# Kernel tuning notes

Measured on AMD Instinct MI355X. Metric: run time of the kernel, lower is better.

## Reference

```python
import jax, jax.numpy as jnp
import numpy as np

E, D, H, R = 8, 2048, 8192, 64   # experts, d_model(in=out), hidden, rank
N = 4096                          # tokens (batch*seq)


def setup_inputs() -> dict:
    key = jax.random.key(0)
    ks = jax.random.split(key, 8)
    f32 = jnp.float32
    x = jax.random.normal(ks[0], (N, D), f32)
    # Stacked low-rank expert params: expert i = relu(x@u1@v1+b1) @ u2 @ v2 + b2
    u1 = jax.random.normal(ks[1], (E, D, R), f32) / np.float32(np.sqrt(D))
    v1 = jax.random.normal(ks[2], (E, R, H), f32) / np.float32(np.sqrt(R))
    b1 = jnp.zeros((E, H), f32)
    u2 = jax.random.normal(ks[3], (E, H, R), f32) / np.float32(np.sqrt(H))
    v2 = jax.random.normal(ks[4], (E, R, D), f32) / np.float32(np.sqrt(R))
    b2 = jnp.zeros((E, D), f32)
    # gate = nn.Linear(D, E): weight [E, D], bias [E]
    gate_w = jax.random.normal(ks[5], (E, D), f32) / np.float32(np.sqrt(D))
    gate_b = jnp.zeros((E,), f32)
    return dict(x=x, u1=u1, v1=v1, b1=b1, u2=u2, v2=v2, b2=b2,
                gate_w=gate_w, gate_b=gate_b)


def reference(x, u1, v1, b1, u2, v2, b2, gate_w, gate_b):
    # --- routing: softmax gate, top-2, renormalize ---
    logits = x @ gate_w.T + gate_b                      # [N, E]
    probs = jax.nn.softmax(logits, axis=-1)
    top_p, top_i = jax.lax.top_k(probs, 2)              # [N, 2]
    top_p = top_p / jnp.sum(top_p, axis=-1, keepdims=True)
    # combine weight per (token, expert): zero unless expert in top-2
    w = jnp.sum(jax.nn.one_hot(top_i, E, dtype=x.dtype) * top_p[..., None], axis=1)  # [N, E]

    # --- experts: low-rank MLP applied per expert, weighted accumulate ---
    def body(acc, params):
        u1e, v1e, b1e, u2e, v2e, b2e, we = params       # we: [N]
        h = jax.nn.relu((x @ u1e) @ v1e + b1e)          # [N, H]
        y = (h @ u2e) @ v2e + b2e                       # [N, D]
        return acc + we[:, None] * y, None

    out, _ = jax.lax.scan(body, jnp.zeros_like(x), (u1, v1, b1, u2, v2, b2, w.T))
    return out
```

## Files before the change

### kernel.cpp

```cpp
#include <hip/hip_runtime.h>
#include <hip/hip_bf16.h>

#define E 8
#define D 2048
#define H 8192
#define R 64
#define NTOK 4096
#define HSPLIT 4
#define HPER (H / HSPLIT)

typedef __attribute__((ext_vector_type(8))) short bf16x8;
typedef __attribute__((ext_vector_type(4))) float f32x4;

__device__ __forceinline__ unsigned short f2b(float f){
  union { __hip_bfloat16 h; unsigned short u; } cv;
  cv.h = __float2bfloat16(f);
  return cv.u;
}
__device__ __forceinline__ float b2f(unsigned short u){
  union { unsigned int i; float f; } cv; cv.i = ((unsigned int)u) << 16; return cv.f;
}

__device__ __forceinline__ bf16x8 ldfrag(const unsigned short* base, int row0, int k0,
                                         int pitch, int lane){
  return *reinterpret_cast<const bf16x8*>(base + (row0 + (lane & 15)) * pitch
                                          + k0 + ((lane >> 4) << 3));
}

__global__ __launch_bounds__(256) void pack_tr(const float* __restrict__ src,
                                               unsigned short* __restrict__ dst,
                                               int RS, int CS){
  int e = blockIdx.z;
  const float* s = src + (size_t)e * RS * CS;
  unsigned short* d = dst + (size_t)e * RS * CS;
  int c0 = blockIdx.x * 64, r0 = blockIdx.y * 64;
  int l = threadIdx.x & 63, cb = (threadIdx.x >> 6) * 16;
  int r = r0 + l;
  const float4* sp = reinterpret_cast<const float4*>(s + (size_t)r * CS + c0 + cb);
  float v[16];
  #pragma unroll
  for (int q = 0; q < 4; ++q){
    float4 t = sp[q];
    v[q*4] = t.x; v[q*4+1] = t.y; v[q*4+2] = t.z; v[q*4+3] = t.w;
  }
  #pragma unroll
  for (int j = 0; j < 16; ++j)
    d[(size_t)(c0 + cb + j) * RS + r] = f2b(v[j]);
}

__global__ __launch_bounds__(256) void gate_kernel(
    const float* __restrict__ x, const float* __restrict__ gw,
    const float* __restrict__ gb, int* __restrict__ tsl,
    unsigned short* __restrict__ xb)
{
  int wid  = threadIdx.x >> 6;
  int lane = threadIdx.x & 63;
  int n0 = blockIdx.x * 8 + wid * 2;

  float acc[2][E];
  #pragma unroll
  for (int t = 0; t < 2; ++t)
    #pragma unroll
    for (int e = 0; e < E; ++e) acc[t][e] = 0.f;

  for (int i = 0; i < D / 256; ++i){
    int dd = i * 256 + lane * 4;
    float4 xv[2];
    #pragma unroll
    for (int t = 0; t < 2; ++t){
      xv[t] = *reinterpret_cast<const float4*>(x + (size_t)(n0 + t) * D + dd);
      unsigned short o[4] = { f2b(xv[t].x), f2b(xv[t].y), f2b(xv[t].z), f2b(xv[t].w) };
      *reinterpret_cast<ushort4*>(xb + (size_t)(n0 + t) * D + dd) = *reinterpret_cast<ushort4*>(o);
    }
    #pragma unroll
    for (int e = 0; e < E; ++e){
      float4 g = *reinterpret_cast<const float4*>(gw + (size_t)e * D + dd);
      #pragma unroll
      for (int t = 0; t < 2; ++t)
        acc[t][e] += xv[t].x * g.x + xv[t].y * g.y + xv[t].z * g.z + xv[t].w * g.w;
    }
  }

  #pragma unroll
  for (int t = 0; t < 2; ++t){
    #pragma unroll
    for (int e = 0; e < E; ++e){
      float v = acc[t][e];
      for (int off = 32; off; off >>= 1) v += __shfl_xor(v, off, 64);
      acc[t][e] = v + gb[e];
    }
    if (lane == 0){
      int n = n0 + t;
      float l0 = -1e30f, l1 = -1e30f; int i0 = 0, i1 = 0;
      #pragma unroll
      for (int e = 0; e < E; ++e){
        float v = acc[t][e];
        if (v > l0){ l1 = l0; i1 = i0; l0 = v; i0 = e; }
        else if (v > l1){ l1 = v; i1 = e; }
      }
      float tt = expf(l1 - l0);
      float w0 = 1.f / (1.f + tt);
      float w1 = tt * w0;
      int* ts = tsl + n * 8;
      ts[0] = i0; ts[2] = __float_as_int(w0);
      ts[3] = i1; ts[5] = __float_as_int(w1);
    }
  }
}

__global__ __launch_bounds__(256) void route_kernel(
    int* __restrict__ tsl, int* __restrict__ cnt, int* __restrict__ lst)
{
  int wid  = threadIdx.x >> 6;
  int lane = threadIdx.x & 63;
  int tok  = blockIdx.x * 256 + wid * 64 + lane;
  int* ts = tsl + tok * 8;
  int i0 = ts[0], i1 = ts[3];
  unsigned long long below = (1ULL << lane) - 1ULL;

  #pragma unroll
  for (int e = 0; e < E; ++e){
    unsigned long long m0 = __ballot(i0 == e);
    unsigned long long m1 = __ballot(i1 == e);
    int c0  = __popcll(m0);
    int tot = c0 + __popcll(m1);
    int base = 0;
    if (lane == 0 && tot) base = atomicAdd(&cnt[e], tot);
    base = __shfl(base, 0, 64);
    if (i0 == e){
      int p = base + __popcll(m0 & below);
      lst[e * NTOK + p] = tok;  ts[1] = p;
    }
    if (i1 == e){
      int p = base + c0 + __popcll(m1 & below);
      lst[e * NTOK + p] = tok;  ts[4] = p;
    }
  }
}

__global__ __launch_bounds__(256) void t1_kernel(
    const unsigned short* __restrict__ xb, const unsigned short* __restrict__ u1p,
    const int* __restrict__ cnt, const int* __restrict__ lst,
    unsigned short* __restrict__ T1buf)
{
  int e = blockIdx.y;
  int nc = cnt[e];
  int t0 = blockIdx.x * 64;
  if (t0 >= nc) return;

  __shared__ int s_tok[64];
  __shared__ unsigned short Xs[64 * 136];
  __shared__ unsigned short U1s[64 * 136];
  int tid = threadIdx.x, w = tid >> 6, lane = tid & 63;

  if (tid < 64) s_tok[tid] = lst[e * NTOK + min(t0 + tid, nc - 1)];
  __syncthreads();

  int m = (w & 3) * 16;
  f32x4 z = {0.f, 0.f, 0.f, 0.f};
  f32x4 acc[4] = {z, z, z, z};

  for (int kc = 0; kc < D; kc += 128){
    __syncthreads();
    #pragma unroll
    for (int s = 0; s < 4; ++s){
      int id = tid + s * 256;
      int rr = id >> 4, c = (id & 15) * 8;
      *reinterpret_cast<bf16x8*>(&Xs[rr * 136 + c]) =
        *reinterpret_cast<const bf16x8*>(&xb[(size_t)s_tok[rr] * D + kc + c]);
      *reinterpret_cast<bf16x8*>(&U1s[rr * 136 + c]) =
        *reinterpret_cast<const bf16x8*>(&u1p[((size_t)e * R + rr) * D + kc + c]);
    }
    __syncthreads();
    #pragma unroll
    for (int j = 0; j < 4; ++j)
      #pragma unroll
      for (int ks = 0; ks < 4; ++ks)
        acc[j] = __builtin_amdgcn_mfma_f32_16x16x32_bf16(
            ldfrag(Xs, m, ks * 32, 136, lane),
            ldfrag(U1s, j * 16, ks * 32, 136, lane), acc[j], 0, 0, 0);
  }
  #pragma unroll
  for (int j = 0; j < 4; ++j){
    int col = j * 16 + (lane & 15);
    #pragma unroll
    for (int q = 0; q < 4; ++q){
      int row = m + ((lane >> 4) << 2) + q;
      T1buf[((size_t)e * NTOK + t0 + row) * R + col] = f2b(acc[j][q]);
    }
  }
}

__global__ __launch_bounds__(512, 4) void mid_kernel(
    const unsigned short* __restrict__ T1buf, const unsigned short* __restrict__ v1p,
    const unsigned short* __restrict__ u2p, const float* __restrict__ b1,
    const int* __restrict__ cnt, float* __restrict__ T2acc)
{
  int e = blockIdx.z;
  int nc = cnt[e];
  int t0 = blockIdx.x * 64;
  if (t0 >= nc) return;
  int hc0 = blockIdx.y * HPER;

  __shared__ unsigned short T1s[64 * 72];
  __shared__ unsigned short v1s[128 * 72];
  __shared__ unsigned short u2s[64 * 136];
  __shared__ unsigned short Hs[64 * 136];
  __shared__ float b1s[HPER];

  int tid = threadIdx.x, w = tid >> 6, lane = tid & 63;

  { int rr = tid >> 3, c = (tid & 7) * 8;
    *reinterpret_cast<bf16x8*>(&T1s[rr * 72 + c]) =
      *reinterpret_cast<const bf16x8*>(&T1buf[((size_t)e * NTOK + t0 + rr) * R + c]); }
  for (int i = tid; i < HPER; i += 512) b1s[i] = b1[(size_t)e * H + hc0 + i];

  int m1 = (w & 1) * 32, n1 = (w >> 1) * 32;
  int m2 = (w & 3) * 16, r2 = (w >> 2) * 32;
  f32x4 z = {0.f, 0.f, 0.f, 0.f};
  f32x4 acc[2] = {z, z};

  bf16x8 pv[2], pu[2];
  #pragma unroll
  for (int s = 0; s < 2; ++s){
    int id = tid + s * 512;
    pv[s] = *reinterpret_cast<const bf16x8*>(&v1p[((size_t)e * H + hc0 + (id >> 3)) * R + (id & 7) * 8]);
    pu[s] = *reinterpret_cast<const bf16x8*>(&u2p[((size_t)e * R + (id >> 4)) * H + hc0 + (id & 15) * 8]);
  }

  for (int hs = 0; hs < HPER; hs += 128){
    __syncthreads();
    #pragma unroll
    for (int s = 0; s < 2; ++s){
      int id = tid + s * 512;
      *reinterpret_cast<bf16x8*>(&v1s[(id >> 3) * 72 + (id & 7) * 8]) = pv[s];
      *reinterpret_cast<bf16x8*>(&u2s[(id >> 4) * 136 + (id & 15) * 8]) = pu[s];
    }
    __syncthreads();
    #pragma unroll
    for (int i = 0; i < 2; ++i)
      #pragma unroll
      for (int j = 0; j < 2; ++j){
        f32x4 a = z;
        #pragma unroll
        for (int ks = 0; ks < 2; ++ks)
          a = __builtin_amdgcn_mfma_f32_16x16x32_bf16(
              ldfrag(T1s, m1 + i * 16, ks * 32, 72, lane),
              ldfrag(v1s, n1 + j * 16, ks * 32, 72, lane), a, 0, 0, 0);
        int hcol = n1 + j * 16 + (lane & 15);
        float bv = b1s[hs + hcol];
        #pragma unroll
        for (int q = 0; q < 4; ++q){
          float vv = a[q] + bv;
          Hs[(m1 + i * 16 + ((lane >> 4) << 2) + q) * 136 + hcol] = f2b(vv > 0.f ? vv : 0.f);
        }
      }
    int hn = (hs + 128 < HPER) ? hs + 128 : 0;
    #pragma unroll
    for (int s = 0; s < 2; ++s){
      int id = tid + s * 512;
      pv[s] = *reinterpret_cast<const bf16x8*>(&v1p[((size_t)e * H + hc0 + hn + (id >> 3)) * R + (id & 7) * 8]);
      pu[s] = *reinterpret_cast<const bf16x8*>(&u2p[((size_t)e * R + (id >> 4)) * H + hc0 + hn + (id & 15) * 8]);
    }
    __syncthreads();
    #pragma unroll
    for (int j = 0; j < 2; ++j)
      #pragma unroll
      for (int ks = 0; ks < 4; ++ks)
        acc[j] = __builtin_amdgcn_mfma_f32_16x16x32_bf16(
            ldfrag(Hs, m2, ks * 32, 136, lane),
            ldfrag(u2s, r2 + j * 16, ks * 32, 136, lane), acc[j], 0, 0, 0);
  }
  #pragma unroll
  for (int j = 0; j < 2; ++j){
    int col = r2 + j * 16 + (lane & 15);
    #pragma unroll
    for (int q = 0; q < 4; ++q){
      int row = m2 + ((lane >> 4) << 2) + q;
      atomicAdd(&T2acc[((size_t)e * NTOK + t0 + row) * R + col], acc[j][q]);
    }
  }
}

__global__ __launch_bounds__(512, 4) void out_kernel(
    const float* __restrict__ T2acc, const unsigned short* __restrict__ v2p,
    const float* __restrict__ b2, const int* __restrict__ cnt,
    unsigned short* __restrict__ yb)
{
  int e = blockIdx.y;
  int nc = cnt[e];
  int t0 = blockIdx.x * 64;
  if (t0 >= nc) return;
  int base = 0;
  #pragma unroll
  for (int i = 0; i < E; ++i) base += (i < e) ? cnt[i] : 0;

  __shared__ unsigned short T2s[64 * 72];
  __shared__ unsigned short v2s[256 * 72];
  __shared__ float b2s[D];
  int tid = threadIdx.x, w = tid >> 6, lane = tid & 63;

  { int rr = tid >> 3, c = (tid & 7) * 8;
    const float* src = &T2acc[((size_t)e * NTOK + t0 + rr) * R + c];
    float4 a = *reinterpret_cast<const float4*>(src);
    float4 b = *reinterpret_cast<const float4*>(src + 4);
    unsigned short o[8] = { f2b(a.x), f2b(a.y), f2b(a.z), f2b(a.w),
                            f2b(b.x), f2b(b.y), f2b(b.z), f2b(b.w) };
    *reinterpret_cast<bf16x8*>(&T2s[rr * 72 + c]) = *reinterpret_cast<bf16x8*>(o); }
  for (int i = tid; i < D; i += 512) b2s[i] = b2[(size_t)e * D + i];

  int m1 = (w & 1) * 32, nb = (w >> 1) * 64;
  f32x4 z = {0.f, 0.f, 0.f, 0.f};

  for (int dc = 0; dc < D; dc += 256){
    __syncthreads();
    #pragma unroll
    for (int s = 0; s < 4; ++s){
      int id = tid + s * 512;
      int rr = id >> 3, c = (id & 7) * 8;
      *reinterpret_cast<bf16x8*>(&v2s[rr * 72 + c]) =
        *reinterpret_cast<const bf16x8*>(&v2p[((size_t)e * D + dc + rr) * R + c]);
    }
    __syncthreads();
    #pragma unroll
    for (int i = 0; i < 2; ++i)
      #pragma unroll
      for (int j = 0; j < 4; ++j){
        f32x4 a = z;
        #pragma unroll
        for (int ks = 0; ks < 2; ++ks)
          a = __builtin_amdgcn_mfma_f32_16x16x32_bf16(
              ldfrag(T2s, m1 + i * 16, ks * 32, 72, lane),
              ldfrag(v2s, nb + j * 16, ks * 32, 72, lane), a, 0, 0, 0);
        int dcol = dc + nb + j * 16 + (lane & 15);
        float bv = b2s[dcol];
        #pragma unroll
        for (int q = 0; q < 4; ++q){
          int row = m1 + i * 16 + ((lane >> 4) << 2) + q;
          if (t0 + row < nc)
            yb[((size_t)(base + t0 + row)) * D + dcol] = f2b(a[q] + bv);
        }
      }
  }
}

__global__ __launch_bounds__(256) void combine_kernel(
    const unsigned short* __restrict__ yb, const int* __restrict__ tsl,
    const int* __restrict__ cnt, float* __restrict__ out)
{
  int tok = blockIdx.x;
  int d0 = threadIdx.x * 8;
  const int* ts = tsl + tok * 8;
  int e0 = ts[0], p0 = ts[1]; float w0 = __int_as_float(ts[2]);
  int e1 = ts[3], p1 = ts[4]; float w1 = __int_as_float(ts[5]);
  int b0 = 0, b1s = 0;
  #pragma unroll
  for (int i = 0; i < E; ++i){
    int c = cnt[i];
    b0  += (i < e0) ? c : 0;
    b1s += (i < e1) ? c : 0;
  }
  bf16x8 y0 = *reinterpret_cast<const bf16x8*>(&yb[((size_t)(b0 + p0)) * D + d0]);
  bf16x8 y1 = *reinterpret_cast<const bf16x8*>(&yb[((size_t)(b1s + p1)) * D + d0]);
  float o[8];
  #pragma unroll
  for (int j = 0; j < 8; ++j)
    o[j] = w0 * b2f((unsigned short)y0[j]) + w1 * b2f((unsigned short)y1[j]);
  *reinterpret_cast<float4*>(&out[(size_t)tok * D + d0])     = *reinterpret_cast<float4*>(&o[0]);
  *reinterpret_cast<float4*>(&out[(size_t)tok * D + d0 + 4]) = *reinterpret_cast<float4*>(&o[4]);
}

extern "C" void kernel_launch(void* const* d_in, const int* in_sizes, int n_in,
                              void* d_out, int out_size, void* d_ws, size_t ws_size,
                              hipStream_t stream)
{
  const float* x  = (const float*)d_in[0];
  const float* u1 = (const float*)d_in[1];
  const float* v1 = (const float*)d_in[2];
  const float* b1 = (const float*)d_in[3];
  const float* u2 = (const float*)d_in[4];
  const float* v2 = (const float*)d_in[5];
  const float* b2 = (const float*)d_in[6];
  const float* gw = (const float*)d_in[7];
  const float* gb = (const float*)d_in[8];
  float* out = (float*)d_out;

  const size_t SZ_XB  = (size_t)NTOK * D * 2;
  const size_t SZ_U1P = (size_t)E * R * D * 2;
  const size_t SZ_V1P = (size_t)E * H * R * 2;
  const size_t SZ_U2P = (size_t)E * R * H * 2;
  const size_t SZ_V2P = (size_t)E * D * R * 2;
  const size_t SZ_T1  = (size_t)E * NTOK * R * 2;
  const size_t SZ_T2  = (size_t)E * NTOK * R * 4;

  char* ws = (char*)d_ws;
  size_t o = 0;
  auto take = [&](size_t b){ void* p = ws + o; o = (o + b + 255) & ~(size_t)255; return p; };
  int* cnt = (int*)take(E * 4);
  int* lst = (int*)take((size_t)E * NTOK * 4);
  int* tsl = (int*)take((size_t)NTOK * 8 * 4);
  char* A  = (char*)take(SZ_XB + SZ_U1P + SZ_V1P + SZ_U2P);
  unsigned short* xb  = (unsigned short*)A;
  unsigned short* u1p = (unsigned short*)(A + SZ_XB);
  unsigned short* v1p = (unsigned short*)(A + SZ_XB + SZ_U1P);
  unsigned short* u2p = (unsigned short*)(A + SZ_XB + SZ_U1P + SZ_V1P);
  unsigned short* yb  = (unsigned short*)A;
  unsigned short* v2p = (unsigned short*)take(SZ_V2P);
  unsigned short* T1buf = (unsigned short*)take(SZ_T1);
  float* T2acc = (float*)take(SZ_T2);

  hipMemsetAsync(cnt, 0, E * 4, stream);
  hipMemsetAsync(T2acc, 0, SZ_T2, stream);

  gate_kernel<<<NTOK / 8, 256, 0, stream>>>(x, gw, gb, tsl, xb);
  route_kernel<<<NTOK / 256, 256, 0, stream>>>(tsl, cnt, lst);
  pack_tr<<<dim3(1, D / 64, E), 256, 0, stream>>>(u1, u1p, D, R);
  pack_tr<<<dim3(H / 64, 1, E), 256, 0, stream>>>(v1, v1p, R, H);
  pack_tr<<<dim3(1, H / 64, E), 256, 0, stream>>>(u2, u2p, H, R);
  pack_tr<<<dim3(D / 64, 1, E), 256, 0, stream>>>(v2, v2p, R, D);

  t1_kernel<<<dim3(NTOK / 64, E), 256, 0, stream>>>(xb, u1p, cnt, lst, T1buf);
  mid_kernel<<<dim3(NTOK / 64, HSPLIT, E), 512, 0, stream>>>(T1buf, v1p, u2p, b1, cnt, T2acc);
  out_kernel<<<dim3(NTOK / 64, E), 512, 0, stream>>>(T2acc, v2p, b2, cnt, yb);
  combine_kernel<<<NTOK, 256, 0, stream>>>(yb, tsl, cnt, out);
}
```

Before: 309.8 us.

## Double mid_kernel token tile to 128 and switch to 32x32x16 MFMA

Each mid_kernel block now handles 128 tokens instead of 64, so every staged v1/u2 weight chunk serves twice as many rows, halving weight traffic per token. The warp mapping is rebuilt around 32x32x16 bf16 MFMAs. In the second GEMM the two warp groups each take half of the 128-wide hidden chunk and both add into T2acc through atomics, which doubles the atomic count. Larger LDS and accumulator use lowers the occupancy hint to 2 blocks per CU, and fewer blocks are launched.

```diff
diff --git a/kernel.cpp b/kernel.cpp
--- a/kernel.cpp
+++ b/kernel.cpp
@@ -8,9 +8,11 @@
 #define NTOK 4096
 #define HSPLIT 4
 #define HPER (H / HSPLIT)
+#define MSLOT 128
 
 typedef __attribute__((ext_vector_type(8))) short bf16x8;
 typedef __attribute__((ext_vector_type(4))) float f32x4;
+typedef __attribute__((ext_vector_type(16))) float f32x16;
 
 __device__ __forceinline__ unsigned short f2b(float f){
   union { __hip_bfloat16 h; unsigned short u; } cv;
@@ -25,6 +27,11 @@
                                          int pitch, int lane){
   return *reinterpret_cast<const bf16x8*>(base + (row0 + (lane & 15)) * pitch
                                           + k0 + ((lane >> 4) << 3));
+}
+__device__ __forceinline__ bf16x8 ldfrag32(const unsigned short* base, int row0, int k0,
+                                           int pitch, int lane){
+  return *reinterpret_cast<const bf16x8*>(base + (row0 + (lane & 31)) * pitch
+                                          + k0 + ((lane >> 5) << 3));
 }
 
 __global__ __launch_bounds__(256) void pack_tr(const float* __restrict__ src,
@@ -191,34 +198,41 @@
   }
 }
 
-__global__ __launch_bounds__(512, 4) void mid_kernel(
+__global__ __launch_bounds__(512, 2) void mid_kernel(
     const unsigned short* __restrict__ T1buf, const unsigned short* __restrict__ v1p,
     const unsigned short* __restrict__ u2p, const float* __restrict__ b1,
     const int* __restrict__ cnt, float* __restrict__ T2acc)
 {
   int e = blockIdx.z;
   int nc = cnt[e];
-  int t0 = blockIdx.x * 64;
+  int t0 = blockIdx.x * MSLOT;
   if (t0 >= nc) return;
   int hc0 = blockIdx.y * HPER;
 
-  __shared__ unsigned short T1s[64 * 72];
+  __shared__ unsigned short T1s[MSLOT * 72];
   __shared__ unsigned short v1s[128 * 72];
   __shared__ unsigned short u2s[64 * 136];
-  __shared__ unsigned short Hs[64 * 136];
+  __shared__ unsigned short Hs[MSLOT * 136];
   __shared__ float b1s[HPER];
 
   int tid = threadIdx.x, w = tid >> 6, lane = tid & 63;
 
-  { int rr = tid >> 3, c = (tid & 7) * 8;
+  #pragma unroll
+  for (int s = 0; s < 2; ++s){
+    int id = tid + s * 512;
+    int rr = id >> 3, c = (id & 7) * 8;
     *reinterpret_cast<bf16x8*>(&T1s[rr * 72 + c]) =
-      *reinterpret_cast<const bf16x8*>(&T1buf[((size_t)e * NTOK + t0 + rr) * R + c]); }
+      *reinterpret_cast<const bf16x8*>(&T1buf[((size_t)e * NTOK + t0 + rr) * R + c]);
+  }
   for (int i = tid; i < HPER; i += 512) b1s[i] = b1[(size_t)e * H + hc0 + i];
 
-  int m1 = (w & 1) * 32, n1 = (w >> 1) * 32;
-  int m2 = (w & 3) * 16, r2 = (w >> 2) * 32;
-  f32x4 z = {0.f, 0.f, 0.f, 0.f};
-  f32x4 acc[2] = {z, z};
+  int mB = (w & 3) * 32;
+  int nB = (w >> 2) * 64;
+  int kh = (w >> 2) * 64;
+
+  f32x16 acc0, acc1;
+  #pragma unroll
+  for (int q = 0; q < 16; ++q){ acc0[q] = 0.f; acc1[q] = 0.f; }
 
   bf16x8 pv[2], pu[2];
   #pragma unroll
@@ -237,24 +251,29 @@
       *reinterpret_cast<bf16x8*>(&u2s[(id >> 4) * 136 + (id & 15) * 8]) = pu[s];
     }
     __syncthreads();
-    #pragma unroll
-    for (int i = 0; i < 2; ++i)
+
+    f32x16 h0, h1;
+    #pragma unroll
+    for (int q = 0; q < 16; ++q){ h0[q] = 0.f; h1[q] = 0.f; }
+    #pragma unroll
+    for (int kc = 0; kc < 4; ++kc){
+      bf16x8 a = ldfrag32(T1s, mB, kc * 16, 72, lane);
+      h0 = __builtin_amdgcn_mfma_f32_32x32x16_bf16(
+          a, ldfrag32(v1s, nB, kc * 16, 72, lane), h0, 0, 0, 0);
+      h1 = __builtin_amdgcn_mfma_f32_32x32x16_bf16(
+          a, ldfrag32(v1s, nB + 32, kc * 16, 72, lane), h1, 0, 0, 0);
+    }
+    {
+      int c0 = nB + (lane & 31);
+      float bv0 = b1s[hs + c0], bv1 = b1s[hs + c0 + 32];
       #pragma unroll
-      for (int j = 0; j < 2; ++j){
-        f32x4 a = z;
-        #pragma unroll
-        for (int ks = 0; ks < 2; ++ks)
-          a = __builtin_amdgcn_mfma_f32_16x16x32_bf16(
-              ldfrag(T1s, m1 + i * 16, ks * 32, 72, lane),
-              ldfrag(v1s, n1 + j * 16, ks * 32, 72, lane), a, 0, 0, 0);
-        int hcol = n1 + j * 16 + (lane & 15);
-        float bv = b1s[hs + hcol];
-        #pragma unroll
-        for (int q = 0; q < 4; ++q){
-          float vv = a[q] + bv;
-          Hs[(m1 + i * 16 + ((lane >> 4) << 2) + q) * 136 + hcol] = f2b(vv > 0.f ? vv : 0.f);
-        }
+      for (int q = 0; q < 16; ++q){
+        int srow = mB + (q & 3) + 8 * (q >> 2) + 4 * (lane >> 5);
+        float v0 = h0[q] + bv0, v1v = h1[q] + bv1;
+        Hs[srow * 136 + c0]      = f2b(v0 > 0.f ? v0 : 0.f);
+        Hs[srow * 136 + c0 + 32] = f2b(v1v > 0.f ? v1v : 0.f);
       }
+    }
     int hn = (hs + 128 < HPER) ? hs + 128 : 0;
     #pragma unroll
     for (int s = 0; s < 2; ++s){
@@ -263,22 +282,24 @@
       pu[s] = *reinterpret_cast<const bf16x8*>(&u2p[((size_t)e * R + (id >> 4)) * H + hc0 + hn + (id & 15) * 8]);
     }
     __syncthreads();
-    #pragma unroll
-    for (int j = 0; j < 2; ++j)
-      #pragma unroll
-      for (int ks = 0; ks < 4; ++ks)
-        acc[j] = __builtin_amdgcn_mfma_f32_16x16x32_bf16(
-            ldfrag(Hs, m2, ks * 32, 136, lane),
-            ldfrag(u2s, r2 + j * 16, ks * 32, 136, lane), acc[j], 0, 0, 0);
-  }
-  #pragma unroll
-  for (int j = 0; j < 2; ++j){
-    int col = r2 + j * 16 + (lane & 15);
-    #pragma unroll
-    for (int q = 0; q < 4; ++q){
-      int row = m2 + ((lane >> 4) << 2) + q;
-      atomicAdd(&T2acc[((size_t)e * NTOK + t0 + row) * R + col], acc[j][q]);
-    }
+
+    #pragma unroll
+    for (int kc = 0; kc < 4; ++kc){
+      bf16x8 a = ldfrag32(Hs, mB, kh + kc * 16, 136, lane);
+      acc0 = __builtin_amdgcn_mfma_f32_32x32x16_bf16(
+          a, ldfrag32(u2s, 0,  kh + kc * 16, 136, lane), acc0, 0, 0, 0);
+      acc1 = __builtin_amdgcn_mfma_f32_32x32x16_bf16(
+          a, ldfrag32(u2s, 32, kh + kc * 16, 136, lane), acc1, 0, 0, 0);
+    }
+  }
+
+  int col = lane & 31;
+  #pragma unroll
+  for (int q = 0; q < 16; ++q){
+    int srow = mB + (q & 3) + 8 * (q >> 2) + 4 * (lane >> 5);
+    float* dst = &T2acc[((size_t)e * NTOK + t0 + srow) * R];
+    atomicAdd(dst + col,      acc0[q]);
+    atomicAdd(dst + col + 32, acc1[q]);
   }
 }
 
@@ -420,7 +441,7 @@
   pack_tr<<<dim3(D / 64, 1, E), 256, 0, stream>>>(v2, v2p, R, D);
 
   t1_kernel<<<dim3(NTOK / 64, E), 256, 0, stream>>>(xb, u1p, cnt, lst, T1buf);
-  mid_kernel<<<dim3(NTOK / 64, HSPLIT, E), 512, 0, stream>>>(T1buf, v1p, u2p, b1, cnt, T2acc);
+  mid_kernel<<<dim3(NTOK / MSLOT, HSPLIT, E), 512, 0, stream>>>(T1buf, v1p, u2p, b1, cnt, T2acc);
   out_kernel<<<dim3(NTOK / 64, E), 512, 0, stream>>>(T2acc, v2p, b2, cnt, yb);
   combine_kernel<<<NTOK, 256, 0, stream>>>(yb, tsl, cnt, out);
 }
```

New measurement: 342.7 us. 10.6% more time.
